# Kernel optimization log

Hardware: AMD Instinct MI355X
Metric: run time of the kernel (lower is better)

The kernel has to match this reference:

```python
import jax, jax.numpy as jnp
import numpy as np

DIM = 5120
HEADS = 40
HEAD_DIM = DIM // HEADS
EPS = 1e-6


def rms_norm(x, w, eps=EPS):
    var = jnp.mean(jnp.square(x), axis=-1, keepdims=True)
    return x * jax.lax.rsqrt(var + eps) * w


def apply_rotary(x, freqs_cos, freqs_sin):
    # x: [B, L, H, D]; freqs: [1, L, 1, D] (broadcastable)
    x_even = x[..., 0::2]
    x_odd = x[..., 1::2]
    cos_e = freqs_cos[..., 0::2]
    sin_o = freqs_sin[..., 1::2]
    out_even = x_even * cos_e - x_odd * sin_o
    out_odd = x_even * sin_o + x_odd * cos_e
    # interleave back: [..., D//2, 2] -> [..., D]
    return jnp.stack([out_even, out_odd], axis=-1).reshape(x.shape)


def setup_inputs() -> dict:
    key = jax.random.key(0)
    ks = jax.random.split(key, 8)
    B, L = 1, 2048
    scale_in = 1.0 / np.sqrt(DIM)
    return {
        "hidden_states": jax.random.normal(ks[0], (B, L, DIM), jnp.float32),
        "freqs_cos": jax.random.normal(ks[1], (1, L, 1, HEAD_DIM), jnp.float32),
        "freqs_sin": jax.random.normal(ks[2], (1, L, 1, HEAD_DIM), jnp.float32),
        "W_qkv": jax.random.normal(ks[3], (DIM, 3 * DIM), jnp.float32) * scale_in,
        "b_qkv": jnp.zeros((3 * DIM,), jnp.float32),
        "w_norm_q": jnp.ones((DIM,), jnp.float32),
        "w_norm_k": jnp.ones((DIM,), jnp.float32),
        "W_out": jax.random.normal(ks[4], (DIM, DIM), jnp.float32) * scale_in,
        "b_out": jnp.zeros((DIM,), jnp.float32),
    }


def reference(hidden_states, freqs_cos, freqs_sin, W_qkv, b_qkv,
              w_norm_q, w_norm_k, W_out, b_out):
    B, L, D = hidden_states.shape
    qkv = hidden_states @ W_qkv + b_qkv                     # [B, L, 3D]
    q, k, v = jnp.split(qkv, 3, axis=-1)
    q = rms_norm(q, w_norm_q)                               # norm over full dim=5120
    k = rms_norm(k, w_norm_k)
    q = q.reshape(B, L, HEADS, HEAD_DIM)
    k = k.reshape(B, L, HEADS, HEAD_DIM)
    v = v.reshape(B, L, HEADS, HEAD_DIM)
    q = apply_rotary(q, freqs_cos, freqs_sin)
    k = apply_rotary(k, freqs_cos, freqs_sin)
    scale = 1.0 / np.sqrt(HEAD_DIM)
    scores = jnp.einsum("bqhd,bkhd->bhqk", q, k) * scale    # [B, H, L, L]
    attn = jax.nn.softmax(scores, axis=-1)
    out = jnp.einsum("bhqk,bkhd->bqhd", attn, v)            # [B, L, H, D]
    out = out.reshape(B, L, D)
    return out @ W_out + b_out
```

## Files before the change

### kernel.cpp

```cpp
#include <hip/hip_runtime.h>
#include <cstdint>
#include <cstddef>

#define L_C   2048
#define DIMC  5120
#define HD    128
#define NHEADS 40

typedef __bf16 bf16_t;
typedef __bf16 bf16x8 __attribute__((ext_vector_type(8)));
typedef __bf16 bf16x4 __attribute__((ext_vector_type(4)));
typedef float  f32x4  __attribute__((ext_vector_type(4)));

#define MFMA16(A,B,C) __builtin_amdgcn_mfma_f32_16x16x32_bf16((A),(B),(C),0,0,0)
#define BARRIER() __builtin_amdgcn_s_barrier()
#define VMCNT0() asm volatile("s_waitcnt vmcnt(0)" ::: "memory")

__device__ __forceinline__ void gload16(const void* g, void* l) {
  __builtin_amdgcn_global_load_lds(
      (__attribute__((address_space(1))) void*)(void*)g,
      (__attribute__((address_space(3))) void*)l, 16, 0, 0);
}

__global__ __launch_bounds__(256) void f32_to_bf16(const float* __restrict__ in,
                                                   bf16_t* __restrict__ out, size_t n8) {
  size_t i = (size_t)blockIdx.x * blockDim.x + threadIdx.x;
  size_t stride = (size_t)gridDim.x * blockDim.x;
  for (; i < n8; i += stride) {
    f32x4 a = *(const f32x4*)(in + i * 8);
    f32x4 b = *(const f32x4*)(in + i * 8 + 4);
    bf16x8 o;
#pragma unroll
    for (int j = 0; j < 4; ++j) { o[j] = (bf16_t)a[j]; o[4 + j] = (bf16_t)b[j]; }
    *(bf16x8*)(out + i * 8) = o;
  }
}

__global__ __launch_bounds__(256) void wtrans(const float* __restrict__ W,
                                              bf16_t* __restrict__ Wt, int K, int N) {
  __shared__ bf16_t t[64][68];
  const int k0 = blockIdx.x * 64, n0 = blockIdx.y * 64, tid = threadIdx.x;
#pragma unroll
  for (int i = 0; i < 4; ++i) {
    int c = i * 256 + tid, rk = c >> 4, cn = (c & 15) * 4;
    f32x4 v = *(const f32x4*)(W + (size_t)(k0 + rk) * N + n0 + cn);
    bf16x4 o;
#pragma unroll
    for (int j = 0; j < 4; ++j) o[j] = (bf16_t)v[j];
    *(bf16x4*)&t[rk][cn] = o;
  }
  __syncthreads();
#pragma unroll
  for (int i = 0; i < 2; ++i) {
    int c = i * 256 + tid, rn = c >> 3, ck = (c & 7) * 8;
    bf16x8 v;
#pragma unroll
    for (int j = 0; j < 8; ++j) v[j] = t[ck + j][rn];
    *(bf16x8*)(Wt + (size_t)(n0 + rn) * K + k0 + ck) = v;
  }
}

__global__ __launch_bounds__(256) void v_trans(const bf16_t* __restrict__ qkv,
                                               bf16_t* __restrict__ Vt) {
  __shared__ bf16_t t[64][136];
  const int l0 = blockIdx.x * 64, h = blockIdx.y, tid = threadIdx.x;
#pragma unroll
  for (int i = 0; i < 4; ++i) {
    int c = i * 256 + tid, row = c >> 4, cb = c & 15;
    *(bf16x8*)&t[row][cb * 8] =
        *(const bf16x8*)(qkv + (size_t)(l0 + row) * (3 * DIMC) + 2 * DIMC + h * HD + cb * 8);
  }
  __syncthreads();
#pragma unroll
  for (int i = 0; i < 4; ++i) {
    int c = i * 256 + tid, d = c >> 3, lb = c & 7;
    bf16x8 v;
#pragma unroll
    for (int j = 0; j < 8; ++j) v[j] = t[lb * 8 + j][d];
    *(bf16x8*)(Vt + ((size_t)h * HD + d) * L_C + l0 + lb * 8) = v;
  }
}

template <int OUT_BF16, int K>
__global__ __launch_bounds__(512, 1) void gemm8(const bf16_t* __restrict__ A,
                                                const bf16_t* __restrict__ Bt,
                                                const float* __restrict__ bias,
                                                bf16_t* __restrict__ Cb,
                                                float* __restrict__ Cf,
                                                int M, int N) {
  __shared__ __align__(16) char smem[131072];
  const int tid = threadIdx.x;
  const int wid = tid >> 6, lane = tid & 63;
  const int g = lane >> 4, r = lane & 15;
  const int wm = wid >> 2, wn = wid & 3;
  const int nb = gridDim.x * gridDim.y;
  const int bid = blockIdx.y * gridDim.x + blockIdx.x;
  const int swz = (bid & 7) * (nb >> 3) + (bid >> 3);
  const int bm = swz % gridDim.x, bn = swz / gridDim.x;
  const int row0 = bm * 256, col0 = bn * 256;

  auto stageA = [&](int buf, int half, int kt) {
#pragma unroll
    for (int i = 0; i < 2; ++i) {
      const int idx = i * 512 + tid;
      const int rl = idx >> 3, c = idx & 7;
      gload16(A + (size_t)(row0 + half * 128 + rl) * K + kt * 64 + ((c ^ (rl & 7)) << 3),
              smem + buf * 65536 + half * 16384 + (i * 512 + wid * 64) * 16);
    }
  };
  auto stageB = [&](int buf, int half, int kt) {
#pragma unroll
    for (int i = 0; i < 2; ++i) {
      const int idx = i * 512 + tid;
      const int rl = idx >> 3, c = idx & 7;
      gload16(Bt + (size_t)(col0 + half * 128 + rl) * K + kt * 64 + ((c ^ (rl & 7)) << 3),
              smem + buf * 65536 + 32768 + half * 16384 + (i * 512 + wid * 64) * 16);
    }
  };
  auto ldA = [&](int buf, int mi, int kk) {
    const int rh = mi * 16 + r;
    return *(const bf16x8*)(smem + buf * 65536 + wm * 16384 + rh * 128 +
                            (((kk * 4 + g) ^ (r & 7)) << 4));
  };
  auto ldB = [&](int buf, int ni, int kk) {
    const int rh = (wn & 1) * 64 + ni * 16 + r;
    return *(const bf16x8*)(smem + buf * 65536 + 32768 + (wn >> 1) * 16384 + rh * 128 +
                            (((kk * 4 + g) ^ (r & 7)) << 4));
  };

  f32x4 acc[8][4] = {};
  bf16x8 af[4][2], bfr[4][2];
  constexpr int nk = K / 64;

  stageA(0, 0, 0); stageA(0, 1, 0); stageB(0, 0, 0); stageB(0, 1, 0);
  VMCNT0();
  BARRIER();

  auto ktile = [&](int k, int cur) {
    const bool pf = (k + 1 < nk);
#pragma unroll
    for (int i = 0; i < 4; ++i)
#pragma unroll
      for (int kk = 0; kk < 2; ++kk) af[i][kk] = ldA(cur, i, kk);
#pragma unroll
    for (int j = 0; j < 2; ++j)
#pragma unroll
      for (int kk = 0; kk < 2; ++kk) bfr[j][kk] = ldB(cur, j, kk);
    if (pf) { stageA(cur ^ 1, 0, k + 1); stageA(cur ^ 1, 1, k + 1); }
    BARRIER();
    __builtin_amdgcn_s_setprio(1);
#pragma unroll
    for (int i = 0; i < 4; ++i)
#pragma unroll
      for (int j = 0; j < 2; ++j)
#pragma unroll
        for (int kk = 0; kk < 2; ++kk)
          acc[i][j] = MFMA16(af[i][kk], bfr[j][kk], acc[i][j]);
    __builtin_amdgcn_s_setprio(0);
    BARRIER();
#pragma unroll
    for (int j = 0; j < 2; ++j)
#pragma unroll
      for (int kk = 0; kk < 2; ++kk) bfr[2 + j][kk] = ldB(cur, 2 + j, kk);
    if (pf) { stageB(cur ^ 1, 0, k + 1); stageB(cur ^ 1, 1, k + 1); }
    BARRIER();
    __builtin_amdgcn_s_setprio(1);
#pragma unroll
    for (int i = 0; i < 4; ++i)
#pragma unroll
      for (int j = 0; j < 2; ++j)
#pragma unroll
        for (int kk = 0; kk < 2; ++kk)
          acc[i][2 + j] = MFMA16(af[i][kk], bfr[2 + j][kk], acc[i][2 + j]);
    __builtin_amdgcn_s_setprio(0);
    BARRIER();
#pragma unroll
    for (int i = 0; i < 4; ++i)
#pragma unroll
      for (int kk = 0; kk < 2; ++kk) af[i][kk] = ldA(cur, 4 + i, kk);
    BARRIER();
    __builtin_amdgcn_s_setprio(1);
#pragma unroll
    for (int i = 0; i < 4; ++i)
#pragma unroll
      for (int j = 0; j < 2; ++j)
#pragma unroll
        for (int kk = 0; kk < 2; ++kk)
          acc[4 + i][2 + j] = MFMA16(af[i][kk], bfr[2 + j][kk], acc[4 + i][2 + j]);
    __builtin_amdgcn_s_setprio(0);
    BARRIER();
    __builtin_amdgcn_s_setprio(1);
#pragma unroll
    for (int i = 0; i < 4; ++i)
#pragma unroll
      for (int j = 0; j < 2; ++j)
#pragma unroll
        for (int kk = 0; kk < 2; ++kk)
          acc[4 + i][j] = MFMA16(af[i][kk], bfr[j][kk], acc[4 + i][j]);
    __builtin_amdgcn_s_setprio(0);
    VMCNT0();
    BARRIER();
  };

  for (int kp = 0; kp < nk; kp += 2) { ktile(kp, 0); ktile(kp + 1, 1); }

#pragma unroll
  for (int mi = 0; mi < 8; ++mi)
#pragma unroll
    for (int ni = 0; ni < 4; ++ni)
#pragma unroll
      for (int p = 0; p < 4; ++p) {
        const int rr = row0 + wm * 128 + mi * 16 + 4 * g + p;
        const int cc = col0 + wn * 64 + ni * 16 + r;
        const float v = acc[mi][ni][p] + bias[cc];
        if (OUT_BF16) Cb[(size_t)rr * N + cc] = (bf16_t)v;
        else          Cf[(size_t)rr * N + cc] = v;
      }
}

__global__ __launch_bounds__(256) void norm_rope(const bf16_t* __restrict__ qkv,
                                                 const float* __restrict__ wq,
                                                 const float* __restrict__ wk,
                                                 const float* __restrict__ fcos,
                                                 const float* __restrict__ fsin,
                                                 bf16_t* __restrict__ Qo,
                                                 bf16_t* __restrict__ Ko) {
  const int l = blockIdx.x, tid = threadIdx.x;
  const bf16_t* row = qkv + (size_t)l * (3 * DIMC);
  float sq = 0.f, sk = 0.f;
  for (int i = tid; i < DIMC / 8; i += 256) {
    bf16x8 a = *(const bf16x8*)(row + i * 8);
    bf16x8 b = *(const bf16x8*)(row + DIMC + i * 8);
#pragma unroll
    for (int j = 0; j < 8; ++j) {
      float x = (float)a[j]; sq += x * x;
      float y = (float)b[j]; sk += y * y;
    }
  }
#pragma unroll
  for (int off = 32; off; off >>= 1) {
    sq += __shfl_xor(sq, off, 64);
    sk += __shfl_xor(sk, off, 64);
  }
  __shared__ float red[2][4];
  const int wid = tid >> 6, lane = tid & 63;
  if (!lane) { red[0][wid] = sq; red[1][wid] = sk; }
  __syncthreads();
  sq = red[0][0] + red[0][1] + red[0][2] + red[0][3];
  sk = red[1][0] + red[1][1] + red[1][2] + red[1][3];
  const float rq = rsqrtf(sq * (1.f / DIMC) + 1e-6f);
  const float rk = rsqrtf(sk * (1.f / DIMC) + 1e-6f);
  for (int i = tid; i < DIMC / 8; i += 256) {
    const int j0 = i * 8, h = j0 >> 7, d0 = j0 & 127;
    bf16x8 a = *(const bf16x8*)(row + j0);
    bf16x8 b = *(const bf16x8*)(row + DIMC + j0);
    f32x4 cA = *(const f32x4*)(fcos + (size_t)l * HD + d0);
    f32x4 cB = *(const f32x4*)(fcos + (size_t)l * HD + d0 + 4);
    f32x4 sA = *(const f32x4*)(fsin + (size_t)l * HD + d0);
    f32x4 sB = *(const f32x4*)(fsin + (size_t)l * HD + d0 + 4);
    f32x4 wqA = *(const f32x4*)(wq + j0), wqB = *(const f32x4*)(wq + j0 + 4);
    f32x4 wkA = *(const f32x4*)(wk + j0), wkB = *(const f32x4*)(wk + j0 + 4);
    float cc[8], ss[8], qn[8], kn[8];
#pragma unroll
    for (int j = 0; j < 4; ++j) {
      cc[j] = cA[j]; cc[4 + j] = cB[j];
      ss[j] = sA[j]; ss[4 + j] = sB[j];
      qn[j] = (float)a[j] * rq * wqA[j];
      qn[4 + j] = (float)a[4 + j] * rq * wqB[j];
      kn[j] = (float)b[j] * rk * wkA[j];
      kn[4 + j] = (float)b[4 + j] * rk * wkB[j];
    }
    bf16x8 oq, ok;
#pragma unroll
    for (int p = 0; p < 4; ++p) {
      const float c = cc[2 * p], s = ss[2 * p + 1];
      oq[2 * p]     = (bf16_t)(qn[2 * p] * c - qn[2 * p + 1] * s);
      oq[2 * p + 1] = (bf16_t)(qn[2 * p] * s + qn[2 * p + 1] * c);
      ok[2 * p]     = (bf16_t)(kn[2 * p] * c - kn[2 * p + 1] * s);
      ok[2 * p + 1] = (bf16_t)(kn[2 * p] * s + kn[2 * p + 1] * c);
    }
    *(bf16x8*)(Qo + ((size_t)h * L_C + l) * HD + d0) = oq;
    *(bf16x8*)(Ko + ((size_t)h * L_C + l) * HD + d0) = ok;
  }
}

__global__ __launch_bounds__(256, 2) void attn(const bf16_t* __restrict__ Q,
                                               const bf16_t* __restrict__ Kg,
                                               const bf16_t* __restrict__ Vt,
                                               bf16_t* __restrict__ O) {
  __shared__ bf16_t k_lds[64 * HD];
  __shared__ bf16_t v_lds[HD * 64];
  __shared__ bf16_t p_lds[4][2][16 * 72];
  const int tid = threadIdx.x, wid = tid >> 6, lane = tid & 63;
  const int g = lane >> 4, r = lane & 15;
  const int bid = blockIdx.x;
  const int grp = bid & 7, inner = bid >> 3;
  const int h = (inner >> 4) * 8 + grp;
  const int q0 = (inner & 15) * 128 + wid * 32;
  bf16x8 qf[2][4];
#pragma unroll
  for (int rg = 0; rg < 2; ++rg) {
    const bf16_t* qrow = Q + ((size_t)h * L_C + q0 + rg * 16 + r) * HD;
#pragma unroll
    for (int ks = 0; ks < 4; ++ks) qf[rg][ks] = *(const bf16x8*)(qrow + ks * 32 + g * 8);
  }
  f32x4 oacc[2][8] = {};
  float m_i[2][4], l_i[2][4];
#pragma unroll
  for (int rg = 0; rg < 2; ++rg)
#pragma unroll
    for (int p = 0; p < 4; ++p) { m_i[rg][p] = -1e30f; l_i[rg][p] = 0.f; }
  const float scale = 0.08838834764831845f;

  bf16x8 kreg[4], vreg[4];
  auto load_kv = [&](int kv0) {
#pragma unroll
    for (int i = 0; i < 4; ++i) {
      const int c = i * 256 + tid;
      const int krow = c >> 4, kcb = c & 15;
      kreg[i] = *(const bf16x8*)(Kg + ((size_t)h * L_C + kv0 + krow) * HD + kcb * 8);
      const int vrow = c >> 3, vcb = c & 7;
      vreg[i] = *(const bf16x8*)(Vt + ((size_t)h * HD + vrow) * L_C + kv0 + vcb * 8);
    }
  };
  load_kv(0);

  for (int kv0 = 0; kv0 < L_C; kv0 += 64) {
    __syncthreads();
#pragma unroll
    for (int i = 0; i < 4; ++i) {
      const int c = i * 256 + tid;
      const int krow = c >> 4, kcb = c & 15;
      *(bf16x8*)((char*)k_lds + krow * 256 + ((kcb * 16) ^ ((krow & 7) << 4))) = kreg[i];
      const int vrow = c >> 3, vcb = c & 7;
      *(bf16x8*)((char*)v_lds + vrow * 128 + ((vcb * 16) ^ ((vrow & 7) << 4))) = vreg[i];
    }
    if (kv0 + 64 < L_C) load_kv(kv0 + 64);
    __syncthreads();

    float pv[2][4][4];
#pragma unroll
    for (int nf = 0; nf < 4; ++nf) {
      f32x4 s0 = {0.f, 0.f, 0.f, 0.f}, s1 = {0.f, 0.f, 0.f, 0.f};
      const int key = nf * 16 + r;
#pragma unroll
      for (int ks = 0; ks < 4; ++ks) {
        bf16x8 kf = *(const bf16x8*)((const char*)k_lds + key * 256 +
                                     ((ks * 64 + g * 16) ^ ((key & 7) << 4)));
        s0 = MFMA16(qf[0][ks], kf, s0);
        s1 = MFMA16(qf[1][ks], kf, s1);
      }
#pragma unroll
      for (int p = 0; p < 4; ++p) { pv[0][nf][p] = s0[p] * scale; pv[1][nf][p] = s1[p] * scale; }
    }
#pragma unroll
    for (int rg = 0; rg < 2; ++rg) {
      float mnew[4];
#pragma unroll
      for (int p = 0; p < 4; ++p)
        mnew[p] = fmaxf(fmaxf(pv[rg][0][p], pv[rg][1][p]), fmaxf(pv[rg][2][p], pv[rg][3][p]));
#pragma unroll
      for (int m = 1; m < 16; m <<= 1)
#pragma unroll
        for (int p = 0; p < 4; ++p) mnew[p] = fmaxf(mnew[p], __shfl_xor(mnew[p], m, 64));
      float alpha[4], rsum[4];
#pragma unroll
      for (int p = 0; p < 4; ++p) {
        const float mi = fmaxf(m_i[rg][p], mnew[p]);
        alpha[p] = __expf(m_i[rg][p] - mi);
        m_i[rg][p] = mi;
        rsum[p] = 0.f;
      }
#pragma unroll
      for (int nf = 0; nf < 4; ++nf)
#pragma unroll
        for (int p = 0; p < 4; ++p) {
          pv[rg][nf][p] = __expf(pv[rg][nf][p] - m_i[rg][p]);
          rsum[p] += pv[rg][nf][p];
        }
#pragma unroll
      for (int nf = 0; nf < 4; ++nf)
#pragma unroll
        for (int p = 0; p < 4; ++p)
          p_lds[wid][rg][(4 * g + p) * 72 + nf * 16 + r] = (bf16_t)pv[rg][nf][p];
#pragma unroll
      for (int m = 1; m < 16; m <<= 1)
#pragma unroll
        for (int p = 0; p < 4; ++p) rsum[p] += __shfl_xor(rsum[p], m, 64);
#pragma unroll
      for (int p = 0; p < 4; ++p) l_i[rg][p] = l_i[rg][p] * alpha[p] + rsum[p];
#pragma unroll
      for (int nf = 0; nf < 8; ++nf)
#pragma unroll
        for (int p = 0; p < 4; ++p) oacc[rg][nf][p] *= alpha[p];
    }
    bf16x8 pf0[2], pf1[2];
#pragma unroll
    for (int rg = 0; rg < 2; ++rg) {
      pf0[rg] = *(const bf16x8*)&p_lds[wid][rg][r * 72 + 8 * g];
      pf1[rg] = *(const bf16x8*)&p_lds[wid][rg][r * 72 + 32 + 8 * g];
    }
#pragma unroll
    for (int nf = 0; nf < 8; ++nf) {
      const int d = nf * 16 + r;
      bf16x8 vf0 = *(const bf16x8*)((const char*)v_lds + d * 128 +
                                    ((g * 16) ^ ((d & 7) << 4)));
      bf16x8 vf1 = *(const bf16x8*)((const char*)v_lds + d * 128 +
                                    ((64 + g * 16) ^ ((d & 7) << 4)));
#pragma unroll
      for (int rg = 0; rg < 2; ++rg) {
        oacc[rg][nf] = MFMA16(pf0[rg], vf0, oacc[rg][nf]);
        oacc[rg][nf] = MFMA16(pf1[rg], vf1, oacc[rg][nf]);
      }
    }
  }
#pragma unroll
  for (int rg = 0; rg < 2; ++rg)
#pragma unroll
    for (int p = 0; p < 4; ++p) {
      const float inv = 1.f / l_i[rg][p];
      const int rowg = q0 + rg * 16 + 4 * g + p;
#pragma unroll
      for (int nf = 0; nf < 8; ++nf) {
        const int d = nf * 16 + r;
        O[(size_t)rowg * DIMC + h * HD + d] = (bf16_t)(oacc[rg][nf][p] * inv);
      }
    }
}

extern "C" void kernel_launch(void* const* d_in, const int* in_sizes, int n_in,
                              void* d_out, int out_size, void* d_ws, size_t ws_size,
                              hipStream_t stream) {
  const float* hidden = (const float*)d_in[0];
  const float* fcos   = (const float*)d_in[1];
  const float* fsin   = (const float*)d_in[2];
  const float* Wqkv   = (const float*)d_in[3];
  const float* bqkv   = (const float*)d_in[4];
  const float* wnq    = (const float*)d_in[5];
  const float* wnk    = (const float*)d_in[6];
  const float* Wout   = (const float*)d_in[7];
  const float* bout   = (const float*)d_in[8];
  float* out = (float*)d_out;

  char* ws = (char*)d_ws;
  size_t off = 0;
  auto alloc = [&](size_t bytes) {
    void* p = ws + off;
    off += (bytes + 255) & ~(size_t)255;
    return p;
  };
  bf16_t* X   = (bf16_t*)alloc((size_t)L_C * DIMC * 2);
  bf16_t* WQT = (bf16_t*)alloc((size_t)3 * DIMC * DIMC * 2);
  bf16_t* WOT = (bf16_t*)alloc((size_t)DIMC * DIMC * 2);
  bf16_t* QKV = (bf16_t*)alloc((size_t)L_C * 3 * DIMC * 2);
  bf16_t* Qb  = (bf16_t*)alloc((size_t)L_C * DIMC * 2);
  bf16_t* Kb  = (bf16_t*)alloc((size_t)L_C * DIMC * 2);
  bf16_t* VT  = (bf16_t*)alloc((size_t)L_C * DIMC * 2);
  bf16_t* Ob  = X;

  f32_to_bf16<<<2048, 256, 0, stream>>>(hidden, X, (size_t)L_C * DIMC / 8);
  wtrans<<<dim3(DIMC / 64, 3 * DIMC / 64), 256, 0, stream>>>(Wqkv, WQT, DIMC, 3 * DIMC);
  wtrans<<<dim3(DIMC / 64, DIMC / 64), 256, 0, stream>>>(Wout, WOT, DIMC, DIMC);
  gemm8<1, DIMC><<<dim3(L_C / 256, 3 * DIMC / 256), 512, 0, stream>>>(
      X, WQT, bqkv, QKV, nullptr, L_C, 3 * DIMC);
  norm_rope<<<L_C, 256, 0, stream>>>(QKV, wnq, wnk, fcos, fsin, Qb, Kb);
  v_trans<<<dim3(L_C / 64, NHEADS), 256, 0, stream>>>(QKV, VT);
  attn<<<(L_C / 128) * NHEADS, 256, 0, stream>>>(Qb, Kb, VT, Ob);
  gemm8<0, DIMC><<<dim3(L_C / 256, DIMC / 256), 512, 0, stream>>>(
      Ob, WOT, bout, nullptr, out, L_C, DIMC);
}
```

Before: 811.3 us.

## Deepen GEMM prefetch, vectorize transposes, cache norm rows in LDS, add setprio

Result: no change. 803.8 us (-0.9%).

```diff
diff --git a/kernel.cpp b/kernel.cpp
--- a/kernel.cpp
+++ b/kernel.cpp
@@ -15,6 +15,7 @@
 #define MFMA16(A,B,C) __builtin_amdgcn_mfma_f32_16x16x32_bf16((A),(B),(C),0,0,0)
 #define BARRIER() __builtin_amdgcn_s_barrier()
 #define VMCNT0() asm volatile("s_waitcnt vmcnt(0)" ::: "memory")
+#define VMCNT8() asm volatile("s_waitcnt vmcnt(8)" ::: "memory")
 
 __device__ __forceinline__ void gload16(const void* g, void* l) {
   __builtin_amdgcn_global_load_lds(
@@ -38,46 +39,56 @@
 
 __global__ __launch_bounds__(256) void wtrans(const float* __restrict__ W,
                                               bf16_t* __restrict__ Wt, int K, int N) {
-  __shared__ bf16_t t[64][68];
+  __shared__ bf16_t t[64 * 68];
   const int k0 = blockIdx.x * 64, n0 = blockIdx.y * 64, tid = threadIdx.x;
-#pragma unroll
-  for (int i = 0; i < 4; ++i) {
-    int c = i * 256 + tid, rk = c >> 4, cn = (c & 15) * 4;
-    f32x4 v = *(const f32x4*)(W + (size_t)(k0 + rk) * N + n0 + cn);
+  const int tn = tid & 15, tk = tid >> 4;
+  f32x4 v[4];
+#pragma unroll
+  for (int jj = 0; jj < 4; ++jj)
+    v[jj] = *(const f32x4*)(W + (size_t)(k0 + 4 * tk + jj) * N + n0 + 4 * tn);
+#pragma unroll
+  for (int j = 0; j < 4; ++j) {
     bf16x4 o;
 #pragma unroll
-    for (int j = 0; j < 4; ++j) o[j] = (bf16_t)v[j];
-    *(bf16x4*)&t[rk][cn] = o;
+    for (int jj = 0; jj < 4; ++jj) o[jj] = (bf16_t)v[jj][j];
+    *(bf16x4*)&t[(4 * tn + j) * 68 + 4 * tk] = o;
   }
   __syncthreads();
 #pragma unroll
   for (int i = 0; i < 2; ++i) {
     int c = i * 256 + tid, rn = c >> 3, ck = (c & 7) * 8;
-    bf16x8 v;
-#pragma unroll
-    for (int j = 0; j < 8; ++j) v[j] = t[ck + j][rn];
-    *(bf16x8*)(Wt + (size_t)(n0 + rn) * K + k0 + ck) = v;
+    bf16x8 o = *(const bf16x8*)&t[rn * 68 + ck];
+    *(bf16x8*)(Wt + (size_t)(n0 + rn) * K + k0 + ck) = o;
   }
 }
 
 __global__ __launch_bounds__(256) void v_trans(const bf16_t* __restrict__ qkv,
                                                bf16_t* __restrict__ Vt) {
-  __shared__ bf16_t t[64][136];
+  __shared__ bf16_t t[128 * 68];
   const int l0 = blockIdx.x * 64, h = blockIdx.y, tid = threadIdx.x;
+  const int td = tid & 31, tl = tid >> 5;
+#pragma unroll
+  for (int it = 0; it < 2; ++it) {
+    const int lq = tl + it * 8;
+    bf16x4 v[4];
+#pragma unroll
+    for (int jj = 0; jj < 4; ++jj)
+      v[jj] = *(const bf16x4*)(qkv + (size_t)(l0 + 4 * lq + jj) * (3 * DIMC) +
+                               2 * DIMC + h * HD + 4 * td);
+#pragma unroll
+    for (int j = 0; j < 4; ++j) {
+      bf16x4 o;
+#pragma unroll
+      for (int jj = 0; jj < 4; ++jj) o[jj] = v[jj][j];
+      *(bf16x4*)&t[(4 * td + j) * 68 + 4 * lq] = o;
+    }
+  }
+  __syncthreads();
 #pragma unroll
   for (int i = 0; i < 4; ++i) {
-    int c = i * 256 + tid, row = c >> 4, cb = c & 15;
-    *(bf16x8*)&t[row][cb * 8] =
-        *(const bf16x8*)(qkv + (size_t)(l0 + row) * (3 * DIMC) + 2 * DIMC + h * HD + cb * 8);
-  }
-  __syncthreads();
-#pragma unroll
-  for (int i = 0; i < 4; ++i) {
-    int c = i * 256 + tid, d = c >> 3, lb = c & 7;
-    bf16x8 v;
-#pragma unroll
-    for (int j = 0; j < 8; ++j) v[j] = t[lb * 8 + j][d];
-    *(bf16x8*)(Vt + ((size_t)h * HD + d) * L_C + l0 + lb * 8) = v;
+    int c = i * 256 + tid, d = c >> 3, cl = (c & 7) * 8;
+    bf16x8 o = *(const bf16x8*)&t[d * 68 + cl];
+    *(bf16x8*)(Vt + ((size_t)h * HD + d) * L_C + l0 + cl) = o;
   }
 }
 
@@ -133,11 +144,12 @@
   constexpr int nk = K / 64;
 
   stageA(0, 0, 0); stageA(0, 1, 0); stageB(0, 0, 0); stageB(0, 1, 0);
-  VMCNT0();
+  stageA(1, 0, 1); stageA(1, 1, 1); stageB(1, 0, 1); stageB(1, 1, 1);
+  VMCNT8();
   BARRIER();
 
   auto ktile = [&](int k, int cur) {
-    const bool pf = (k + 1 < nk);
+    const bool pf2 = (k + 2 < nk);
 #pragma unroll
     for (int i = 0; i < 4; ++i)
 #pragma unroll
@@ -146,7 +158,6 @@
     for (int j = 0; j < 2; ++j)
 #pragma unroll
       for (int kk = 0; kk < 2; ++kk) bfr[j][kk] = ldB(cur, j, kk);
-    if (pf) { stageA(cur ^ 1, 0, k + 1); stageA(cur ^ 1, 1, k + 1); }
     BARRIER();
     __builtin_amdgcn_s_setprio(1);
 #pragma unroll
@@ -162,7 +173,6 @@
     for (int j = 0; j < 2; ++j)
 #pragma unroll
       for (int kk = 0; kk < 2; ++kk) bfr[2 + j][kk] = ldB(cur, 2 + j, kk);
-    if (pf) { stageB(cur ^ 1, 0, k + 1); stageB(cur ^ 1, 1, k + 1); }
     BARRIER();
     __builtin_amdgcn_s_setprio(1);
 #pragma unroll
@@ -178,6 +188,7 @@
     for (int i = 0; i < 4; ++i)
 #pragma unroll
       for (int kk = 0; kk < 2; ++kk) af[i][kk] = ldA(cur, 4 + i, kk);
+    if (pf2) { stageB(cur, 0, k + 2); stageB(cur, 1, k + 2); }
     BARRIER();
     __builtin_amdgcn_s_setprio(1);
 #pragma unroll
@@ -189,6 +200,7 @@
           acc[4 + i][2 + j] = MFMA16(af[i][kk], bfr[2 + j][kk], acc[4 + i][2 + j]);
     __builtin_amdgcn_s_setprio(0);
     BARRIER();
+    if (pf2) { stageA(cur, 0, k + 2); stageA(cur, 1, k + 2); }
     __builtin_amdgcn_s_setprio(1);
 #pragma unroll
     for (int i = 0; i < 4; ++i)
@@ -198,7 +210,7 @@
         for (int kk = 0; kk < 2; ++kk)
           acc[4 + i][j] = MFMA16(af[i][kk], bfr[j][kk], acc[4 + i][j]);
     __builtin_amdgcn_s_setprio(0);
-    VMCNT0();
+    if (pf2) { VMCNT8(); } else { VMCNT0(); }
     BARRIER();
   };
 
@@ -225,12 +237,15 @@
                                                  const float* __restrict__ fsin,
                                                  bf16_t* __restrict__ Qo,
                                                  bf16_t* __restrict__ Ko) {
+  __shared__ bf16_t qs[DIMC], ks_[DIMC];
   const int l = blockIdx.x, tid = threadIdx.x;
   const bf16_t* row = qkv + (size_t)l * (3 * DIMC);
   float sq = 0.f, sk = 0.f;
   for (int i = tid; i < DIMC / 8; i += 256) {
     bf16x8 a = *(const bf16x8*)(row + i * 8);
     bf16x8 b = *(const bf16x8*)(row + DIMC + i * 8);
+    *(bf16x8*)&qs[i * 8] = a;
+    *(bf16x8*)&ks_[i * 8] = b;
 #pragma unroll
     for (int j = 0; j < 8; ++j) {
       float x = (float)a[j]; sq += x * x;
@@ -252,8 +267,8 @@
   const float rk = rsqrtf(sk * (1.f / DIMC) + 1e-6f);
   for (int i = tid; i < DIMC / 8; i += 256) {
     const int j0 = i * 8, h = j0 >> 7, d0 = j0 & 127;
-    bf16x8 a = *(const bf16x8*)(row + j0);
-    bf16x8 b = *(const bf16x8*)(row + DIMC + j0);
+    bf16x8 a = *(const bf16x8*)&qs[j0];
+    bf16x8 b = *(const bf16x8*)&ks_[j0];
     f32x4 cA = *(const f32x4*)(fcos + (size_t)l * HD + d0);
     f32x4 cB = *(const f32x4*)(fcos + (size_t)l * HD + d0 + 4);
     f32x4 sA = *(const f32x4*)(fsin + (size_t)l * HD + d0);
@@ -339,6 +354,7 @@
     __syncthreads();
 
     float pv[2][4][4];
+    __builtin_amdgcn_s_setprio(1);
 #pragma unroll
     for (int nf = 0; nf < 4; ++nf) {
       f32x4 s0 = {0.f, 0.f, 0.f, 0.f}, s1 = {0.f, 0.f, 0.f, 0.f};
@@ -353,6 +369,7 @@
 #pragma unroll
       for (int p = 0; p < 4; ++p) { pv[0][nf][p] = s0[p] * scale; pv[1][nf][p] = s1[p] * scale; }
     }
+    __builtin_amdgcn_s_setprio(0);
 #pragma unroll
     for (int rg = 0; rg < 2; ++rg) {
       float mnew[4];
@@ -400,6 +417,7 @@
       pf0[rg] = *(const bf16x8*)&p_lds[wid][rg][r * 72 + 8 * g];
       pf1[rg] = *(const bf16x8*)&p_lds[wid][rg][r * 72 + 32 + 8 * g];
     }
+    __builtin_amdgcn_s_setprio(1);
 #pragma unroll
     for (int nf = 0; nf < 8; ++nf) {
       const int d = nf * 16 + r;
@@ -413,6 +431,7 @@
         oacc[rg][nf] = MFMA16(pf1[rg], vf1, oacc[rg][nf]);
       }
     }
+    __builtin_amdgcn_s_setprio(0);
   }
 #pragma unroll
   for (int rg = 0; rg < 2; ++rg)
```
